# Optimization experiments

Hardware: AMD Instinct MI355X
Metric: run time of the kernel (lower is better)

Reference implementation:

```python
import jax, jax.numpy as jnp
import numpy as np
from jax import lax

BETA = 10.0  # undeclared global softmax temperature in the source
STRIDE = 1
PADDING = 1


def setup_inputs() -> dict:
    key = jax.random.key(0)
    k1, k2 = jax.random.split(key)
    B, Ci, Co, K, L = 32, 256, 256, 3, 7  # num_level_conv=8 -> L=7
    x = jax.random.normal(k1, (B, Ci, 56, 56), dtype=jnp.float32)
    p_c = jax.random.normal(k2, (Co, Ci, K, K, L), dtype=jnp.float32)
    # reset_parameters with num_level=8, s=1: t1=4, t2=floor(log2(1))=0,
    # t3=arange(-2,1)=[-2,-1,0] -> q_level = sort(-2**t3) ++ [0] ++ 2**t3
    t3 = np.arange(-2, 1, dtype=np.float32)
    q_level = jnp.asarray(
        np.concatenate([np.sort(-(2.0 ** t3)), np.zeros(1, np.float32), 2.0 ** t3]),
        dtype=jnp.float32,
    )
    return {"x": x, "p_c": p_c, "q_level": q_level}


def reference(x, p_c, q_level):
    # soft quantization of the conv weight
    norm = jnp.sqrt(jnp.sum(p_c * p_c, axis=-1, keepdims=True))  # (O,I,K,K,1)
    s_c = jax.nn.softmax(BETA * (p_c / norm), axis=-1)           # (O,I,K,K,L)
    conv_w = jnp.einsum("oihwl,l->oihw", s_c, q_level)           # (O,I,K,K)
    # the source's double loop over (kh,kw) with strided slicing + matmul
    # is exactly stride-S cross-correlation with zero padding
    out = lax.conv_general_dilated(
        x,
        conv_w,
        window_strides=(STRIDE, STRIDE),
        padding=[(PADDING, PADDING), (PADDING, PADDING)],
        dimension_numbers=("NCHW", "OIHW", "NCHW"),
    )
    return out
```

## Files before the change

### kernel.cpp

```cpp
#include <hip/hip_runtime.h>
#include <math.h>

#define CI   256
#define CO   256
#define HW   56
#define LQ   7
#define BETA 10.0f

typedef __attribute__((ext_vector_type(8))) short short8;
typedef __attribute__((ext_vector_type(4))) float f32x4;

__device__ __forceinline__ ushort f2bf(float f) {
    uint u = __float_as_uint(f);
    u += 0x7FFF + ((u >> 16) & 1);
    return (ushort)(u >> 16);
}

__global__ void quant_weights(const float* __restrict__ p_c,
                              const float* __restrict__ q_level,
                              short* __restrict__ W2) {
    int idx = blockIdx.x * blockDim.x + threadIdx.x;
    if (idx >= CO * CI) return;
    int co = idx >> 8, ci = idx & 255;
    float ql[LQ];
#pragma unroll
    for (int l = 0; l < LQ; ++l) ql[l] = q_level[l];
    const float* p = p_c + (size_t)idx * 9 * LQ;
#pragma unroll
    for (int t = 0; t < 9; ++t) {
        float pv[LQ];
        float ss = 0.f;
#pragma unroll
        for (int l = 0; l < LQ; ++l) { pv[l] = p[t * LQ + l]; ss += pv[l] * pv[l]; }
        float inv = rsqrtf(ss) * BETA;
        float m = -1e30f;
#pragma unroll
        for (int l = 0; l < LQ; ++l) { pv[l] *= inv; m = fmaxf(m, pv[l]); }
        float den = 0.f, num = 0.f;
#pragma unroll
        for (int l = 0; l < LQ; ++l) {
            float e = expf(pv[l] - m);
            den += e;
            num += e * ql[l];
        }
        float val = num / den;
        int widx = ((((ci >> 5) * 9 + t) * 4 + ((ci >> 3) & 3)) * 2048) + co * 8 + (ci & 7);
        W2[widx] = (short)f2bf(val);
    }
}

__global__ __launch_bounds__(256, 2) void conv_mfma(const float* __restrict__ x,
                                                    const short* __restrict__ W2,
                                                    float* __restrict__ out) {
    __shared__ __align__(16) short xt[6 * 72 * 32];

    const int tid  = threadIdx.x;
    const int lane = tid & 63;
    const int wv   = tid >> 6;
    const int l15  = lane & 15;
    const int kb   = lane >> 4;
    const int wm    = (wv >> 1) * 64;
    const int wnrow = (wv & 1) * 2;

    const int h0  = blockIdx.x * 4;
    const int co0 = blockIdx.y * 128;
    const int b   = blockIdx.z;

    f32x4 acc[4][8];
#pragma unroll
    for (int a = 0; a < 4; ++a)
#pragma unroll
        for (int f = 0; f < 8; ++f) acc[a][f] = (f32x4){0.f, 0.f, 0.f, 0.f};

    const float* xb = x + (size_t)b * CI * HW * HW;

    for (int ch = 0; ch < 8; ++ch) {
        const int ci0 = ch * 32;
        for (int f = tid; f < 6 * 66; f += 256) {
            int r = f / 66, c = f % 66;
            int h = h0 - 1 + r, wc = c - 1;
            bool valid = (h >= 0) & (h < HW) & (wc >= 0) & (wc < HW);
            const float* xs = xb + (size_t)ci0 * 3136 + (valid ? (h * HW + wc) : 0);
            int sw = (c >> 1) & 3;
            int sbase = (r * 72 + c) * 32;
#pragma unroll
            for (int k = 0; k < 4; ++k) {
                short8 pk;
#pragma unroll
                for (int e = 0; e < 8; ++e) {
                    float v = xs[(size_t)(k * 8 + e) * 3136];
                    pk[e] = (short)f2bf(valid ? v : 0.f);
                }
                *(short8*)&xt[sbase + ((k ^ sw) * 8)] = pk;
            }
        }
        __syncthreads();

#pragma unroll
        for (int kh = 0; kh < 3; ++kh) {
#pragma unroll
            for (int kw = 0; kw < 3; ++kw) {
                const int t = kh * 3 + kw;
                const short* ap = W2 + (size_t)((((ch * 9 + t) * 4 + kb) * 256) + co0 + wm + l15) * 8;
                short8 af[4];
#pragma unroll
                for (int a = 0; a < 4; ++a) af[a] = *(const short8*)(ap + a * 128);

                const int c0 = kw + l15;
                const int r0 = wnrow + kh;
                const short* bp = &xt[(r0 * 72 + c0) * 32 + ((kb ^ ((c0 >> 1) & 3)) * 8)];
                short8 bf[8];
#pragma unroll
                for (int f = 0; f < 8; ++f)
                    bf[f] = *(const short8*)(bp + (f >> 2) * 2304 + (f & 3) * 512);

#pragma unroll
                for (int a = 0; a < 4; ++a)
#pragma unroll
                    for (int f = 0; f < 8; ++f)
                        acc[a][f] = __builtin_amdgcn_mfma_f32_16x16x32_bf16(af[a], bf[f], acc[a][f], 0, 0, 0);
            }
        }
        __syncthreads();
    }

#pragma unroll
    for (int a = 0; a < 4; ++a) {
#pragma unroll
        for (int f = 0; f < 8; ++f) {
            int wloc = (f & 3) * 16 + l15;
            if (wloc < HW) {
                int h = h0 + wnrow + (f >> 2);
#pragma unroll
                for (int j = 0; j < 4; ++j) {
                    int cog = co0 + wm + 16 * a + kb * 4 + j;
                    out[(((size_t)b * CO + cog) * HW + h) * HW + wloc] = acc[a][f][j];
                }
            }
        }
    }
}

extern "C" void kernel_launch(void* const* d_in, const int* in_sizes, int n_in,
                              void* d_out, int out_size, void* d_ws, size_t ws_size,
                              hipStream_t stream) {
    const float* x       = (const float*)d_in[0];
    const float* p_c     = (const float*)d_in[1];
    const float* q_level = (const float*)d_in[2];
    float* out = (float*)d_out;
    short* W2  = (short*)d_ws;

    quant_weights<<<(CO * CI + 255) / 256, 256, 0, stream>>>(p_c, q_level, W2);

    dim3 grid(HW / 4, CO / 128, 32);
    conv_mfma<<<grid, 256, 0, stream>>>(x, W2, out);
}
```

Before: 166.0 us.

## Pre-transpose input to padded NHWC bf16 and double-buffer LDS via direct global-to-LDS loads

Adds prep kernels that convert x once into a zero-padded NHWC bf16 buffer in workspace. The conv kernel then streams channel chunks straight into a double-buffered LDS tile with global_load_lds and explicit waitcnt, overlapping the next chunk's load with the MFMA work on the current one. Previously every block gathered strided fp32 values, converted them and stored them itself, and both co-blocks of a batch repeated that work. The cost is an extra global read and write of the whole input, two more launches, and a dependence on workspace size, with the old kernel kept as a fallback.

```diff
diff --git a/kernel.cpp b/kernel.cpp
--- a/kernel.cpp
+++ b/kernel.cpp
@@ -49,10 +49,60 @@
     }
 }
 
-__global__ __launch_bounds__(256, 2) void conv_mfma(const float* __restrict__ x,
-                                                    const short* __restrict__ W2,
-                                                    float* __restrict__ out) {
-    __shared__ __align__(16) short xt[6 * 72 * 32];
+__global__ void prep_border(ushort* __restrict__ xt) {
+    int idx = blockIdx.x * 256 + threadIdx.x;
+    int b = blockIdx.y;
+    if (idx >= 228 * 32) return;
+    int pos = idx >> 5, chk = idx & 31;
+    int hh, ww;
+    if (pos < 58)       { hh = 0;  ww = pos; }
+    else if (pos < 116) { hh = 57; ww = pos - 58; }
+    else { int q = pos - 116; hh = 1 + (q >> 1); ww = (q & 1) ? 57 : 0; }
+    size_t o = (((size_t)b * 58 + hh) * 58 + ww) * 256 + chk * 8;
+    uint4 z = {0, 0, 0, 0};
+    *(uint4*)&xt[o] = z;
+}
+
+__global__ __launch_bounds__(256) void prep_main(const float* __restrict__ x,
+                                                 ushort* __restrict__ xt) {
+    __shared__ ushort ld[256 * 60];
+    const int tid = threadIdx.x;
+    const int h = blockIdx.x;
+    const int b = blockIdx.y;
+    const float* xp = x + ((size_t)b * CI) * 3136 + h * HW;
+#pragma unroll
+    for (int s = 0; s < 14; ++s) {
+        int flat = s * 1024 + tid * 4;
+        int ci = flat / 56;
+        int w  = flat - ci * 56;
+        const float4 v = *(const float4*)(xp + (size_t)ci * 3136 + w);
+        ushort4 o;
+        o.x = f2bf(v.x); o.y = f2bf(v.y); o.z = f2bf(v.z); o.w = f2bf(v.w);
+        *(ushort4*)&ld[ci * 60 + w] = o;
+    }
+    __syncthreads();
+    const int w = tid & 63;
+    const int wq = tid >> 6;
+    if (w < 56) {
+        size_t obase = (((size_t)b * 58 + h + 1) * 58 + (w + 1)) * 256;
+#pragma unroll
+        for (int s = 0; s < 8; ++s) {
+            int cig = s * 4 + wq;
+            int base = (cig * 8) * 60 + w;
+            uint u0 = (uint)ld[base]       | ((uint)ld[base + 60]  << 16);
+            uint u1 = (uint)ld[base + 120] | ((uint)ld[base + 180] << 16);
+            uint u2 = (uint)ld[base + 240] | ((uint)ld[base + 300] << 16);
+            uint u3 = (uint)ld[base + 360] | ((uint)ld[base + 420] << 16);
+            uint4 o = {u0, u1, u2, u3};
+            *(uint4*)&xt[obase + cig * 8] = o;
+        }
+    }
+}
+
+__global__ __launch_bounds__(256, 2) void conv_mfma2(const ushort* __restrict__ xt_g,
+                                                     const short* __restrict__ W2,
+                                                     float* __restrict__ out) {
+    __shared__ __align__(16) ushort xt[2][12672];
 
     const int tid  = threadIdx.x;
     const int lane = tid & 63;
@@ -66,6 +116,117 @@
     const int co0 = blockIdx.y * 128;
     const int b   = blockIdx.z;
 
+    int src_off[7];
+#pragma unroll
+    for (int s = 0; s < 7; ++s) {
+        int gl = s * 64 + lane;
+        int gg = wv * 396 + (gl < 396 ? gl : 0);
+        int kbq = gg & 3, pos = gg >> 2;
+        int r = pos / 66, c = pos - r * 66;
+        int wp = c < 58 ? c : 57;
+        int ci = (kbq ^ ((c >> 1) & 3)) << 3;
+        src_off[s] = ((b * 58 + h0 + r) * 58 + wp) * 256 + ci;
+    }
+
+    f32x4 acc[4][8];
+#pragma unroll
+    for (int a = 0; a < 4; ++a)
+#pragma unroll
+        for (int f = 0; f < 8; ++f) acc[a][f] = (f32x4){0.f, 0.f, 0.f, 0.f};
+
+    {
+        const ushort* sp = xt_g;
+        ushort* lb = &xt[0][wv * 396 * 8];
+#pragma unroll
+        for (int s = 0; s < 7; ++s) {
+            if (s * 64 + lane < 396)
+                __builtin_amdgcn_global_load_lds(
+                    (const __attribute__((address_space(1))) void*)(sp + src_off[s]),
+                    (__attribute__((address_space(3))) void*)(lb + s * 512), 16, 0, 0);
+        }
+    }
+
+    for (int ch = 0; ch < 8; ++ch) {
+        if (ch < 7) {
+            const ushort* sp = xt_g + (ch + 1) * 32;
+            ushort* lb = &xt[(ch + 1) & 1][wv * 396 * 8];
+#pragma unroll
+            for (int s = 0; s < 7; ++s) {
+                if (s * 64 + lane < 396)
+                    __builtin_amdgcn_global_load_lds(
+                        (const __attribute__((address_space(1))) void*)(sp + src_off[s]),
+                        (__attribute__((address_space(3))) void*)(lb + s * 512), 16, 0, 0);
+            }
+            asm volatile("s_waitcnt vmcnt(7)" ::: "memory");
+        } else {
+            asm volatile("s_waitcnt vmcnt(0)" ::: "memory");
+        }
+        __builtin_amdgcn_s_barrier();
+
+        const ushort* buf = xt[ch & 1];
+#pragma unroll
+        for (int kh = 0; kh < 3; ++kh) {
+#pragma unroll
+            for (int kw = 0; kw < 3; ++kw) {
+                const int t = kh * 3 + kw;
+                const short* ap = W2 + (size_t)(((ch * 9 + t) * 4 + kb) * 256 + co0 + wm + l15) * 8;
+                short8 af[4];
+#pragma unroll
+                for (int a = 0; a < 4; ++a) af[a] = *(const short8*)(ap + a * 128);
+
+                const int c0 = kw + l15;
+                const int r0 = wnrow + kh;
+                const ushort* bp = &buf[((r0 * 66 + c0) * 4 + (kb ^ ((c0 >> 1) & 3))) * 8];
+                short8 bf[8];
+#pragma unroll
+                for (int f = 0; f < 8; ++f)
+                    bf[f] = *(const short8*)(bp + (f >> 2) * 2112 + (f & 3) * 512);
+
+#pragma unroll
+                for (int a = 0; a < 4; ++a)
+#pragma unroll
+                    for (int f = 0; f < 8; ++f)
+                        acc[a][f] = __builtin_amdgcn_mfma_f32_16x16x32_bf16(af[a], bf[f], acc[a][f], 0, 0, 0);
+            }
+        }
+        asm volatile("s_waitcnt lgkmcnt(0)" ::: "memory");
+        __builtin_amdgcn_s_barrier();
+    }
+
+#pragma unroll
+    for (int a = 0; a < 4; ++a) {
+#pragma unroll
+        for (int f = 0; f < 8; ++f) {
+            int wloc = (f & 3) * 16 + l15;
+            if (wloc < HW) {
+                int h = h0 + wnrow + (f >> 2);
+#pragma unroll
+                for (int j = 0; j < 4; ++j) {
+                    int cog = co0 + wm + 16 * a + kb * 4 + j;
+                    out[(((size_t)b * CO + cog) * HW + h) * HW + wloc] = acc[a][f][j];
+                }
+            }
+        }
+    }
+}
+
+__global__ __launch_bounds__(256, 2) void conv_mfma_fb(const float* __restrict__ x,
+                                                       const short* __restrict__ W2,
+                                                       float* __restrict__ out) {
+    __shared__ __align__(16) short xs[6 * 72 * 32];
+
+    const int tid  = threadIdx.x;
+    const int lane = tid & 63;
+    const int wv   = tid >> 6;
+    const int l15  = lane & 15;
+    const int kb   = lane >> 4;
+    const int wm    = (wv >> 1) * 64;
+    const int wnrow = (wv & 1) * 2;
+
+    const int h0  = blockIdx.x * 4;
+    const int co0 = blockIdx.y * 128;
+    const int b   = blockIdx.z;
+
     f32x4 acc[4][8];
 #pragma unroll
     for (int a = 0; a < 4; ++a)
@@ -80,7 +241,7 @@
             int r = f / 66, c = f % 66;
             int h = h0 - 1 + r, wc = c - 1;
             bool valid = (h >= 0) & (h < HW) & (wc >= 0) & (wc < HW);
-            const float* xs = xb + (size_t)ci0 * 3136 + (valid ? (h * HW + wc) : 0);
+            const float* xsrc = xb + (size_t)ci0 * 3136 + (valid ? (h * HW + wc) : 0);
             int sw = (c >> 1) & 3;
             int sbase = (r * 72 + c) * 32;
 #pragma unroll
@@ -88,10 +249,10 @@
                 short8 pk;
 #pragma unroll
                 for (int e = 0; e < 8; ++e) {
-                    float v = xs[(size_t)(k * 8 + e) * 3136];
+                    float v = xsrc[(size_t)(k * 8 + e) * 3136];
                     pk[e] = (short)f2bf(valid ? v : 0.f);
                 }
-                *(short8*)&xt[sbase + ((k ^ sw) * 8)] = pk;
+                *(short8*)&xs[sbase + ((k ^ sw) * 8)] = pk;
             }
         }
         __syncthreads();
@@ -108,7 +269,7 @@
 
                 const int c0 = kw + l15;
                 const int r0 = wnrow + kh;
-                const short* bp = &xt[(r0 * 72 + c0) * 32 + ((kb ^ ((c0 >> 1) & 3)) * 8)];
+                const short* bp = &xs[(r0 * 72 + c0) * 32 + ((kb ^ ((c0 >> 1) & 3)) * 8)];
                 short8 bf[8];
 #pragma unroll
                 for (int f = 0; f < 8; ++f)
@@ -148,10 +309,19 @@
     const float* p_c     = (const float*)d_in[1];
     const float* q_level = (const float*)d_in[2];
     float* out = (float*)d_out;
-    short* W2  = (short*)d_ws;
+
+    short* W2 = (short*)d_ws;
+    const size_t XT_OFF = 2u * 1024 * 1024;
+    const size_t need = XT_OFF + (size_t)32 * 3364 * 256 * 2;
 
     quant_weights<<<(CO * CI + 255) / 256, 256, 0, stream>>>(p_c, q_level, W2);
 
-    dim3 grid(HW / 4, CO / 128, 32);
-    conv_mfma<<<grid, 256, 0, stream>>>(x, W2, out);
-}
+    if (ws_size >= need) {
+        ushort* xt_g = (ushort*)((char*)d_ws + XT_OFF);
+        prep_border<<<dim3(29, 32), 256, 0, stream>>>(xt_g);
+        prep_main<<<dim3(56, 32), 256, 0, stream>>>(x, xt_g);
+        conv_mfma2<<<dim3(14, 2, 32), 256, 0, stream>>>(xt_g, W2, out);
+    } else {
+        conv_mfma_fb<<<dim3(14, 2, 32), 256, 0, stream>>>(x, W2, out);
+    }
+}
```

After: 181.4 us. 9.3% more time.
